# Kernel tuning notes

Hardware: AMD Instinct MI355X
Metric: run time of the kernel (lower is better)

The kernel has to match this reference:

```python
import jax, jax.numpy as jnp
import numpy as np

LOG2 = float(np.log(2.0))

def _ssp(x):
    # shifted softplus: ln(0.5*(exp(x)+1)) = softplus(x) - ln 2
    return jax.nn.softplus(x) - LOG2

def setup_inputs() -> dict:
    key = jax.random.key(0)
    ks = jax.random.split(key, 8)
    B, N, D = 32, 512, 1024
    H = D // 2
    s = lambda fan_in: 1.0 / np.sqrt(fan_in)
    return {
        "representation": jax.random.normal(ks[0], (B, N, D), jnp.float32),
        "R": jax.random.normal(ks[1], (B, N, 3), jnp.float32),
        "atom_mask": jnp.ones((B, N), jnp.float32),
        "W1": jax.random.normal(ks[2], (D, H), jnp.float32) * s(D),
        "b1": jnp.zeros((H,), jnp.float32),
        "W2": jax.random.normal(ks[3], (H, 1), jnp.float32) * s(H),
        "b2": jnp.zeros((1,), jnp.float32),
        "Wc1": jax.random.normal(ks[4], (D, H), jnp.float32) * s(D),
        "bc1": jnp.zeros((H,), jnp.float32),
        "Wc2": jax.random.normal(ks[5], (H, 1), jnp.float32) * s(H),
        "bc2": jnp.zeros((1,), jnp.float32),
    }

def reference(representation, R, atom_mask, W1, b1, W2, b2, Wc1, bc1, Wc2, bc2):
    B, N, _ = representation.shape
    # Atomwise pyramidal MLP: n_in -> n_in//2 (shifted softplus) -> 1
    yi = _ssp(jnp.einsum("bnd,dh->bnh", representation, W1) + b1)
    yi = jnp.einsum("bnh,ho->bno", yi, W2) + b2            # [B,N,1]
    # masked sum pool over atoms (mean=0, stddev=1 so standardize is identity)
    y = jnp.sum(yi * atom_mask[..., None], axis=1)          # [B,1]

    # pairwise distances with safe sqrt (diag is exactly zero)
    diff = R[:, None, :, :] - R[:, :, None, :]              # [B,N,N,3]
    d2 = jnp.sum(diff * diff, axis=-1)                      # [B,N,N]
    dist = jnp.where(d2 > 0, jnp.sqrt(jnp.where(d2 > 0, d2, 1.0)), 0.0)

    eye = jnp.eye(N, dtype=dist.dtype)
    tot_mask = atom_mask[:, None, :] * atom_mask[:, :, None] * (1.0 - eye)
    keep = (tot_mask != 0).astype(dist.dtype)               # [B,N,N]
    dist = dist * keep

    # charge net: Dense(n_in, n_in//2, ssp) -> Dense(n_in//2, 1)
    q = _ssp(jnp.einsum("bnd,dh->bnh", representation, Wc1) + bc1)
    q = jnp.einsum("bnh,ho->bno", q, Wc2) + bc2             # [B,N,1]

    inv2 = (1e-5 + dist) ** -2                              # [B,N,N]
    coulomb = q[:, :, 0][:, None, :] * inv2 * q             # [B,N,N] (q_j * inv * q_i)
    coulomb = coulomb * keep
    e = jnp.sum(coulomb, axis=(1, 2))                       # [B]

    return y + e[:, None]                                   # [B,1]
```

## Files before the change

### kernel.cpp

```cpp
#include <hip/hip_runtime.h>
#include <math.h>


typedef unsigned short u16;
typedef unsigned int u32;
typedef __bf16 bf16x8 __attribute__((ext_vector_type(8)));
typedef float f32x4 __attribute__((ext_vector_type(4)));

#define GK 1024
#define NT 16

#define GLOAD_LDS16(g, l) __builtin_amdgcn_global_load_lds( \
    (const __attribute__((address_space(1))) void*)(g),     \
    (__attribute__((address_space(3))) void*)(l), 16, 0, 0)

__device__ __forceinline__ u16 f2bf(float f) {
    u32 u = __float_as_uint(f);
    return (u16)((u + 0x7FFFu + ((u >> 16) & 1u)) >> 16);
}

__device__ __forceinline__ float ssp_f(float x) {
    return __logf(0.5f * (__expf(x) + 1.0f));
}

__device__ __forceinline__ float ssp_slow(float x) {
    return fmaxf(x, 0.0f) + log1pf(expf(-fabsf(x))) - 0.6931471805599453f;
}


__global__ __launch_bounds__(256) void prep(
    const float* __restrict__ rep, const float* __restrict__ W1,
    const float* __restrict__ Wc1, u16* __restrict__ Abf,
    u16* __restrict__ Btb, float* __restrict__ out)
{
    __shared__ float tile[32][33];
    const int blk = blockIdx.x;
    const int t = threadIdx.x;
    if (blk < 8192) {
        int i = (blk * 256 + t) * 8;
        float4 x = *(const float4*)(rep + i);
        float4 y = *(const float4*)(rep + i + 4);
        union { u16 h[8]; uint4 v; } o;
        o.h[0] = f2bf(x.x); o.h[1] = f2bf(x.y); o.h[2] = f2bf(x.z); o.h[3] = f2bf(x.w);
        o.h[4] = f2bf(y.x); o.h[5] = f2bf(y.y); o.h[6] = f2bf(y.z); o.h[7] = f2bf(y.w);
        *(uint4*)(Abf + i) = o.v;
        if (blk == 0 && t < 32) out[t] = 0.0f;
    } else {
        const int bb = blk - 8192;
        const int k0 = (bb & 31) * 32;
        const int n0 = (bb >> 5) * 32;
        const float* src = (n0 < 512) ? W1 : Wc1;
        const int ns0 = (n0 < 512) ? n0 : n0 - 512;
#pragma unroll
        for (int j = 0; j < 4; j++) {
            int idx = j * 256 + t;
            int kl = idx >> 5, nl = idx & 31;
            tile[kl][nl] = src[(size_t)(k0 + kl) * 512 + ns0 + nl];
        }
        __syncthreads();
#pragma unroll
        for (int j = 0; j < 4; j++) {
            int idx = j * 256 + t;
            int nl = idx >> 5, kl = idx & 31;
            Btb[(size_t)(n0 + nl) * 1024 + k0 + kl] = f2bf(tile[kl][nl]);
        }
    }
}


__global__ __launch_bounds__(512, 2) void gemm_mfma(
    const u16* __restrict__ A,
    const u16* __restrict__ Bt,
    const float* __restrict__ b1, const float* __restrict__ W2,
    const float* __restrict__ bc1, const float* __restrict__ Wc2,
    float* __restrict__ parts)
{
    __shared__ u16 smem[2][16384];

    const int blk = blockIdx.x;
    const int swz = ((blk & 7) << 5) | (blk >> 3);
    const int bm = swz >> 2;
    const int bn = swz & 3;
    const int tid = threadIdx.x;
    const int w = tid >> 6, lane = tid & 63;
    const int wm = w & 1, wn = w >> 1;
    const int lm = lane & 15, q = lane >> 4;

    f32x4 acc[8][4];
#pragma unroll
    for (int i = 0; i < 8; i++)
#pragma unroll
        for (int j = 0; j < 4; j++)
            acc[i][j] = (f32x4){0.0f, 0.0f, 0.0f, 0.0f};

    int goff[2][2];
#pragma unroll
    for (int h = 0; h < 2; h++)
#pragma unroll
        for (int p2 = 0; p2 < 2; p2++) {
            int ci = h * 1024 + (w * 2 + p2) * 64 + lane;
            int row = ci >> 3;
            int c = (ci & 7) ^ (row & 7);
            goff[h][p2] = row * GK + c * 8;
        }

    int arow[4], aswz[2];
#pragma unroll
    for (int mi = 0; mi < 4; mi++) arow[mi] = (wm * 128 + mi * 16 + lm) * 64;
#pragma unroll
    for (int kk = 0; kk < 2; kk++) aswz[kk] = ((kk * 4 + q) ^ (lm & 7)) * 8;

    const u16* Ab = A + (size_t)bm * 256 * GK;
    const u16* Bw = Bt + (size_t)(bn * 256 + wn * 64 + lm) * GK + q * 8;

#define STAGE_A(G, H, BUF) do {                                               \
    GLOAD_LDS16((G) + goff[H][0], &smem[BUF][((H) * 1024 + (w * 2 + 0) * 64) * 8]); \
    GLOAD_LDS16((G) + goff[H][1], &smem[BUF][((H) * 1024 + (w * 2 + 1) * 64) * 8]); \
} while (0)

#define LOAD_B(DST, KT)                                                       \
    _Pragma("unroll") for (int nj = 0; nj < 4; nj++)                          \
    _Pragma("unroll") for (int kk = 0; kk < 2; kk++)                          \
        DST[nj][kk] = *(const bf16x8*)&Bw[(size_t)nj * 16 * GK + (KT) + kk * 32];

#define READ_A(BUF, MH)                                                       \
    _Pragma("unroll") for (int mi = 0; mi < 4; mi++)                          \
    _Pragma("unroll") for (int kk = 0; kk < 2; kk++)                          \
        afr[mi][kk] = *(const bf16x8*)&smem[BUF][arow[mi] + (MH) * 4096 + aswz[kk]];

#define MFMA_HALF(MH, BF)                                                     \
    _Pragma("unroll") for (int kk = 0; kk < 2; kk++)                          \
    _Pragma("unroll") for (int mi = 0; mi < 4; mi++)                          \
    _Pragma("unroll") for (int nj = 0; nj < 4; nj++)                          \
        acc[(MH) * 4 + mi][nj] = __builtin_amdgcn_mfma_f32_16x16x32_bf16(     \
            afr[mi][kk], BF[nj][kk], acc[(MH) * 4 + mi][nj], 0, 0, 0);

#define TILE_BODY(CUR, BCUR, BNXT, TNEXT_KT) do {                             \
    const u16* gA_ = Ab + (TNEXT_KT);                                         \
    STAGE_A(gA_, 0, (CUR) ^ 1);                                               \
    STAGE_A(gA_, 1, (CUR) ^ 1);                                               \
    LOAD_B(BNXT, (TNEXT_KT));                                                 \
    READ_A(CUR, 0);                                                           \
    __builtin_amdgcn_s_setprio(1);                                            \
    MFMA_HALF(0, BCUR);                                                       \
    __builtin_amdgcn_s_setprio(0);                                            \
    READ_A(CUR, 1);                                                           \
    __builtin_amdgcn_s_setprio(1);                                            \
    MFMA_HALF(1, BCUR);                                                       \
    __builtin_amdgcn_s_setprio(0);                                            \
    asm volatile("s_waitcnt vmcnt(0) lgkmcnt(0)" ::: "memory");               \
    __builtin_amdgcn_s_barrier();                                             \
} while (0)

    bf16x8 afr[4][2], bA[4][2], bB[4][2];

    STAGE_A(Ab, 0, 0);
    STAGE_A(Ab, 1, 0);
    LOAD_B(bA, 0);
    asm volatile("s_waitcnt vmcnt(0)" ::: "memory");
    __builtin_amdgcn_s_barrier();

    for (int tt = 0; tt < NT / 2; ++tt) {
        const int t0 = 2 * tt, t1 = 2 * tt + 1;
        TILE_BODY(0, bA, bB, (((t0 + 1) & (NT - 1)) * 64));
        TILE_BODY(1, bB, bA, (((t1 + 1) & (NT - 1)) * 64));
    }

#undef STAGE_A
#undef LOAD_B
#undef READ_A
#undef MFMA_HALF
#undef TILE_BODY

    __syncthreads();
    float* red = (float*)&smem[0][0];
    const bool is_q = (bn >= 2);
    const float* bb2 = is_q ? bc1 : b1;
    const float* vv = is_q ? Wc2 : W2;
    float bias[4], v[4];
#pragma unroll
    for (int nfr = 0; nfr < 4; nfr++) {
        int c = (bn & 1) * 256 + wn * 64 + nfr * 16 + lm;
        bias[nfr] = bb2[c];
        v[nfr] = vv[c];
    }
#pragma unroll
    for (int mfr = 0; mfr < 8; mfr++) {
#pragma unroll
        for (int r = 0; r < 4; r++) {
            float s = 0.0f;
#pragma unroll
            for (int nfr = 0; nfr < 4; nfr++)
                s += v[nfr] * ssp_f(acc[mfr][nfr][r] + bias[nfr]);
            s += __shfl_xor(s, 1);
            s += __shfl_xor(s, 2);
            s += __shfl_xor(s, 4);
            s += __shfl_xor(s, 8);
            if (lm == 0) red[wn * 256 + wm * 128 + mfr * 16 + q * 4 + r] = s;
        }
    }
    __syncthreads();
    if (tid < 256) {
        float val = red[0 * 256 + tid] + red[1 * 256 + tid] +
                    red[2 * 256 + tid] + red[3 * 256 + tid];
        parts[(size_t)bn * 16384 + bm * 256 + tid] = val;
    }
}


__global__ __launch_bounds__(256) void coulomb_k(
    const float* __restrict__ R, const float* __restrict__ mask,
    const float* __restrict__ parts, const float* __restrict__ b2p,
    const float* __restrict__ bc2p, float* __restrict__ out)
{
    const int N = 512;
    const int b = blockIdx.y;
    const int chunk = blockIdx.x;
    __shared__ float Rx[512], Ry[512], Rz[512], QM[512];
    __shared__ float rbuf[4];
    const int tid = threadIdx.x;
    const float bc2 = bc2p[0];
    const float b2 = b2p[0];

    for (int j = tid; j < N; j += 256) {
        int idx = b * N + j;
        float m = mask[idx];
        const float* rp = R + (size_t)idx * 3;
        Rx[j] = rp[0];
        Ry[j] = rp[1];
        Rz[j] = rp[2];
        float qv = parts[2 * 16384 + idx] + parts[3 * 16384 + idx] + bc2;
        QM[j] = qv * m;
    }
    __syncthreads();

    const int i = chunk * 64 + (tid & 63);
    const int js = (tid >> 6) * 128;
    const float xi = Rx[i], yi = Ry[i], zi = Rz[i], qmi = QM[i];
    float e = 0.0f;
    for (int j = js; j < js + 128; j++) {
        float dx = xi - Rx[j];
        float dy = yi - Ry[j];
        float dz = zi - Rz[j];
        float d2 = dx * dx + dy * dy + dz * dz;
        float t = 1e-5f + sqrtf(d2);
        float term = qmi * QM[j] / (t * t);
        e += (j == i) ? 0.0f : term;
    }
    if (tid < 64) {
        int ii = b * N + chunk * 64 + tid;
        float yv = parts[0 * 16384 + ii] + parts[1 * 16384 + ii] + b2;
        e += yv * mask[ii];
    }
    for (int off = 32; off > 0; off >>= 1) e += __shfl_down(e, off, 64);
    if ((tid & 63) == 0) rbuf[tid >> 6] = e;
    __syncthreads();
    if (tid == 0) atomicAdd(&out[b], rbuf[0] + rbuf[1] + rbuf[2] + rbuf[3]);
}


#define BM 128
#define BN 64
#define BK 16

__global__ __launch_bounds__(256) void mlp_gemm(
    const float* __restrict__ A, const float* __restrict__ W1,
    const float* __restrict__ Wc1, const float* __restrict__ b1,
    const float* __restrict__ bc1, const float* __restrict__ W2,
    const float* __restrict__ Wc2, float* __restrict__ yi_part,
    float* __restrict__ q_part)
{
    const int K = 1024;
    const int bm = blockIdx.x;
    const int bn = blockIdx.y;
    const bool is_q = (bn >= 8);
    const float* __restrict__ W = is_q ? Wc1 : W1;
    const int j0 = (bn & 7) * BN;

    __shared__ float As[BK][BM + 4];
    __shared__ float Bs[BK][BN + 4];
    __shared__ float red[BM];

    const int tid = threadIdx.x;
    const int tx = tid & 15;
    const int ty = tid >> 4;

    float acc[8][4];
#pragma unroll
    for (int r = 0; r < 8; r++)
#pragma unroll
        for (int c = 0; c < 4; c++) acc[r][c] = 0.0f;

    const int a_row = tid >> 2;
    const int a_k4 = (tid & 3) * 4;
    const float* Arow0 = A + (size_t)(bm * BM + a_row) * K;
    const float* Arow1 = Arow0 + (size_t)64 * K;
    const int w_k = tid >> 4;
    const int w_j = (tid & 15) * 4;

    for (int kt = 0; kt < K; kt += BK) {
        float4 av0 = *(const float4*)(Arow0 + kt + a_k4);
        float4 av1 = *(const float4*)(Arow1 + kt + a_k4);
        float4 wv = *(const float4*)(W + (size_t)(kt + w_k) * 512 + j0 + w_j);
        __syncthreads();
        As[a_k4 + 0][a_row] = av0.x;
        As[a_k4 + 1][a_row] = av0.y;
        As[a_k4 + 2][a_row] = av0.z;
        As[a_k4 + 3][a_row] = av0.w;
        As[a_k4 + 0][a_row + 64] = av1.x;
        As[a_k4 + 1][a_row + 64] = av1.y;
        As[a_k4 + 2][a_row + 64] = av1.z;
        As[a_k4 + 3][a_row + 64] = av1.w;
        *(float4*)&Bs[w_k][w_j] = wv;
        __syncthreads();
#pragma unroll
        for (int kk = 0; kk < BK; kk++) {
            float4 a0 = *(const float4*)&As[kk][ty * 8];
            float4 a1 = *(const float4*)&As[kk][ty * 8 + 4];
            float4 bv = *(const float4*)&Bs[kk][tx * 4];
            float ar[8] = {a0.x, a0.y, a0.z, a0.w, a1.x, a1.y, a1.z, a1.w};
            float bc[4] = {bv.x, bv.y, bv.z, bv.w};
#pragma unroll
            for (int r = 0; r < 8; r++)
#pragma unroll
                for (int c = 0; c < 4; c++)
                    acc[r][c] = fmaf(ar[r], bc[c], acc[r][c]);
        }
    }

    const float* bb = is_q ? bc1 : b1;
    const float* vv = is_q ? Wc2 : W2;
    float bias[4], v[4];
#pragma unroll
    for (int c = 0; c < 4; c++) {
        bias[c] = bb[j0 + tx * 4 + c];
        v[c] = vv[j0 + tx * 4 + c];
    }
    if (tid < BM) red[tid] = 0.0f;
    __syncthreads();
#pragma unroll
    for (int r = 0; r < 8; r++) {
        float s = 0.0f;
#pragma unroll
        for (int c = 0; c < 4; c++)
            s += v[c] * ssp_slow(acc[r][c] + bias[c]);
        atomicAdd(&red[ty * 8 + r], s);
    }
    __syncthreads();
    float* target = is_q ? q_part : yi_part;
    if (tid < BM) atomicAdd(&target[(size_t)bm * BM + tid], red[tid]);
}

__global__ __launch_bounds__(256) void coulomb_fb(
    const float* __restrict__ R, const float* __restrict__ mask,
    const float* __restrict__ yi_part, const float* __restrict__ q_part,
    const float* __restrict__ b2p, const float* __restrict__ bc2p,
    float* __restrict__ out)
{
    const int N = 512;
    const int b = blockIdx.y;
    const int chunk = blockIdx.x;
    __shared__ float Rx[512], Ry[512], Rz[512], QM[512];
    __shared__ float rbuf[4];
    const int tid = threadIdx.x;
    const float bc2 = bc2p[0];
    const float b2 = b2p[0];

    for (int j = tid; j < N; j += 256) {
        float m = mask[b * N + j];
        const float* rp = R + ((size_t)b * N + j) * 3;
        Rx[j] = rp[0];
        Ry[j] = rp[1];
        Rz[j] = rp[2];
        QM[j] = (q_part[b * N + j] + bc2) * m;
    }
    __syncthreads();

    const int i = chunk * 64 + (tid & 63);
    const int js = (tid >> 6) * 128;
    const float xi = Rx[i], yi = Ry[i], zi = Rz[i], qmi = QM[i];
    float e = 0.0f;
    for (int j = js; j < js + 128; j++) {
        float dx = xi - Rx[j];
        float dy = yi - Ry[j];
        float dz = zi - Rz[j];
        float d2 = dx * dx + dy * dy + dz * dz;
        float t = 1e-5f + sqrtf(d2);
        float term = qmi * QM[j] / (t * t);
        e += (j == i) ? 0.0f : term;
    }
    if (tid < 64) {
        int ii = chunk * 64 + tid;
        e += (yi_part[b * N + ii] + b2) * mask[b * N + ii];
    }
    for (int off = 32; off > 0; off >>= 1) e += __shfl_down(e, off, 64);
    if ((tid & 63) == 0) rbuf[tid >> 6] = e;
    __syncthreads();
    if (tid == 0) atomicAdd(&out[b], rbuf[0] + rbuf[1] + rbuf[2] + rbuf[3]);
}


extern "C" void kernel_launch(void* const* d_in, const int* in_sizes, int n_in,
                              void* d_out, int out_size, void* d_ws, size_t ws_size,
                              hipStream_t stream) {
    const float* rep  = (const float*)d_in[0];
    const float* R    = (const float*)d_in[1];
    const float* mask = (const float*)d_in[2];
    const float* W1   = (const float*)d_in[3];
    const float* b1   = (const float*)d_in[4];
    const float* W2   = (const float*)d_in[5];
    const float* b2   = (const float*)d_in[6];
    const float* Wc1  = (const float*)d_in[7];
    const float* bc1  = (const float*)d_in[8];
    const float* Wc2  = (const float*)d_in[9];
    const float* bc2  = (const float*)d_in[10];
    float* out = (float*)d_out;

    const size_t szA = 16384ull * 1024 * 2;
    const size_t szB = 1024ull * 1024 * 2;
    const size_t szP = 8ull * 16384 * 4;
    const size_t need = szA + szB + szP;

    if (ws_size >= need) {
        u16* Abf = (u16*)d_ws;
        u16* Btb = (u16*)((char*)d_ws + szA);
        float* parts = (float*)((char*)d_ws + szA + szB);

        prep<<<8192 + 1024, 256, 0, stream>>>(rep, W1, Wc1, Abf, Btb, out);
        gemm_mfma<<<256, 512, 0, stream>>>(Abf, Btb, b1, W2, bc1, Wc2, parts);
        coulomb_k<<<dim3(8, 32), 256, 0, stream>>>(R, mask, parts, b2, bc2, out);
    } else {
        float* yi_part = (float*)d_ws;
        float* q_part = yi_part + 16384;
        hipMemsetAsync(d_ws, 0, 2 * 16384 * sizeof(float), stream);
        hipMemsetAsync(d_out, 0, 32 * sizeof(float), stream);
        mlp_gemm<<<dim3(128, 16), 256, 0, stream>>>(rep, W1, Wc1, b1, bc1, W2, Wc2,
                                                    yi_part, q_part);
        coulomb_fb<<<dim3(8, 32), 256, 0, stream>>>(R, mask, yi_part, q_part, b2, bc2, out);
    }
}
```

Baseline: 188.5 us.

## Stage B operand through LDS and pipeline GEMM in quarter-tile phases

The MFMA GEMM now loads the B tile into LDS with async global-to-LDS copies instead of per-wave direct global register loads, and doubles shared memory to hold A and B double buffers. The K-tile body is split into three phases with fine-grained vmcnt/lgkmcnt waits, inline ds_read_b128 with immediate offsets, and barriers, so LDS reads and MFMAs overlap the next tile's staging. The goal is to cut redundant global traffic for B and hide latency. In exchange it uses 128 KB of LDS per block, which may limit occupancy below the declared two blocks per CU, and adds more barriers per tile.

```diff
diff --git a/kernel.cpp b/kernel.cpp
--- a/kernel.cpp
+++ b/kernel.cpp
@@ -75,7 +75,7 @@
     const float* __restrict__ bc1, const float* __restrict__ Wc2,
     float* __restrict__ parts)
 {
-    __shared__ u16 smem[2][16384];
+    __shared__ u16 smem[2][32768];
 
     const int blk = blockIdx.x;
     const int swz = ((blk & 7) << 5) | (blk >> 3);
@@ -93,84 +93,139 @@
         for (int j = 0; j < 4; j++)
             acc[i][j] = (f32x4){0.0f, 0.0f, 0.0f, 0.0f};
 
-    int goff[2][2];
+    int goffA[2][2], goffB[2][2];
 #pragma unroll
     for (int h = 0; h < 2; h++)
 #pragma unroll
         for (int p2 = 0; p2 < 2; p2++) {
             int ci = h * 1024 + (w * 2 + p2) * 64 + lane;
-            int row = ci >> 3;
-            int c = (ci & 7) ^ (row & 7);
-            goff[h][p2] = row * GK + c * 8;
+            int s = ci >> 3;
+            int c = (ci & 7) ^ (s & 7);
+            int gA = (s & 63) + ((s >> 6) & 1) * 128 + ((s >> 7) & 1) * 64;
+            int gB = (s & 31) + ((s >> 5) & 3) * 64 + ((s >> 7) & 1) * 32;
+            goffA[h][p2] = gA * GK + c * 8;
+            goffB[h][p2] = gB * GK + c * 8;
         }
 
-    int arow[4], aswz[2];
-#pragma unroll
-    for (int mi = 0; mi < 4; mi++) arow[mi] = (wm * 128 + mi * 16 + lm) * 64;
-#pragma unroll
-    for (int kk = 0; kk < 2; kk++) aswz[kk] = ((kk * 4 + q) ^ (lm & 7)) * 8;
+    const int aswz0 = (q ^ (lm & 7)) * 8;
+    const int aswz1 = ((4 + q) ^ (lm & 7)) * 8;
+    const u32 base0 = (u32)(size_t)(__attribute__((address_space(3))) void*)&smem[0][0];
+    const u32 aA0 = base0 + 2u * (u32)((wm * 64 + lm) * 64 + aswz0);
+    const u32 aA1 = base0 + 2u * (u32)((wm * 64 + lm) * 64 + aswz1);
+    const u32 bB0 = base0 + 32768u + 2u * (u32)((wn * 32 + lm) * 64 + aswz0);
+    const u32 bB1 = base0 + 32768u + 2u * (u32)((wn * 32 + lm) * 64 + aswz1);
+    const u32 aA0b = aA0 + 65536u, aA1b = aA1 + 65536u;
+    const u32 bB0b = bB0 + 65536u, bB1b = bB1 + 65536u;
 
     const u16* Ab = A + (size_t)bm * 256 * GK;
-    const u16* Bw = Bt + (size_t)(bn * 256 + wn * 64 + lm) * GK + q * 8;
-
-#define STAGE_A(G, H, BUF) do {                                               \
-    GLOAD_LDS16((G) + goff[H][0], &smem[BUF][((H) * 1024 + (w * 2 + 0) * 64) * 8]); \
-    GLOAD_LDS16((G) + goff[H][1], &smem[BUF][((H) * 1024 + (w * 2 + 1) * 64) * 8]); \
+    const u16* Bb = Bt + (size_t)bn * 256 * GK;
+
+#define STAGE2(G, RG, H, BUF, GOFF) do {                                      \
+    GLOAD_LDS16((G) + GOFF[H][0], &smem[BUF][(RG) + ((H) * 1024 + (w * 2 + 0) * 64) * 8]); \
+    GLOAD_LDS16((G) + GOFF[H][1], &smem[BUF][(RG) + ((H) * 1024 + (w * 2 + 1) * 64) * 8]); \
 } while (0)
 
-#define LOAD_B(DST, KT)                                                       \
-    _Pragma("unroll") for (int nj = 0; nj < 4; nj++)                          \
-    _Pragma("unroll") for (int kk = 0; kk < 2; kk++)                          \
-        DST[nj][kk] = *(const bf16x8*)&Bw[(size_t)nj * 16 * GK + (KT) + kk * 32];
-
-#define READ_A(BUF, MH)                                                       \
-    _Pragma("unroll") for (int mi = 0; mi < 4; mi++)                          \
-    _Pragma("unroll") for (int kk = 0; kk < 2; kk++)                          \
-        afr[mi][kk] = *(const bf16x8*)&smem[BUF][arow[mi] + (MH) * 4096 + aswz[kk]];
-
-#define MFMA_HALF(MH, BF)                                                     \
+#define DSR(D, AD, O) asm volatile("ds_read_b128 %0, %1 offset:" #O          \
+                                   : "=v"(D) : "v"(AD))
+
+#define RD_A0(F, R0, R1) do {                                                 \
+    DSR(F[0][0], R0, 0);     DSR(F[0][1], R1, 0);                             \
+    DSR(F[1][0], R0, 2048);  DSR(F[1][1], R1, 2048);                          \
+    DSR(F[2][0], R0, 4096);  DSR(F[2][1], R1, 4096);                          \
+    DSR(F[3][0], R0, 6144);  DSR(F[3][1], R1, 6144); } while (0)
+
+#define RD_A1(F, R0, R1) do {                                                 \
+    DSR(F[0][0], R0, 16384); DSR(F[0][1], R1, 16384);                         \
+    DSR(F[1][0], R0, 18432); DSR(F[1][1], R1, 18432);                         \
+    DSR(F[2][0], R0, 20480); DSR(F[2][1], R1, 20480);                         \
+    DSR(F[3][0], R0, 22528); DSR(F[3][1], R1, 22528); } while (0)
+
+#define RD_B0(F, R0, R1) do {                                                 \
+    DSR(F[0][0], R0, 0);     DSR(F[0][1], R1, 0);                             \
+    DSR(F[1][0], R0, 2048);  DSR(F[1][1], R1, 2048); } while (0)
+
+#define RD_B1(F, R0, R1) do {                                                 \
+    DSR(F[0][0], R0, 16384); DSR(F[0][1], R1, 16384);                         \
+    DSR(F[1][0], R0, 18432); DSR(F[1][1], R1, 18432); } while (0)
+
+#define MFMA_Q(MH, NH, AF, BF)                                                \
     _Pragma("unroll") for (int kk = 0; kk < 2; kk++)                          \
     _Pragma("unroll") for (int mi = 0; mi < 4; mi++)                          \
-    _Pragma("unroll") for (int nj = 0; nj < 4; nj++)                          \
-        acc[(MH) * 4 + mi][nj] = __builtin_amdgcn_mfma_f32_16x16x32_bf16(     \
-            afr[mi][kk], BF[nj][kk], acc[(MH) * 4 + mi][nj], 0, 0, 0);
-
-#define TILE_BODY(CUR, BCUR, BNXT, TNEXT_KT) do {                             \
-    const u16* gA_ = Ab + (TNEXT_KT);                                         \
-    STAGE_A(gA_, 0, (CUR) ^ 1);                                               \
-    STAGE_A(gA_, 1, (CUR) ^ 1);                                               \
-    LOAD_B(BNXT, (TNEXT_KT));                                                 \
-    READ_A(CUR, 0);                                                           \
+    _Pragma("unroll") for (int nj = 0; nj < 2; nj++)                          \
+        acc[(MH) * 4 + mi][(NH) * 2 + nj] = __builtin_amdgcn_mfma_f32_16x16x32_bf16( \
+            AF[mi][kk], BF[nj][kk], acc[(MH) * 4 + mi][(NH) * 2 + nj], 0, 0, 0);
+
+#define WAITV4 do { asm volatile("s_waitcnt vmcnt(4)" ::: "memory");          \
+                    __builtin_amdgcn_sched_barrier(0); } while (0)
+#define LGKM0  do { asm volatile("s_waitcnt lgkmcnt(0)" ::: "memory");        \
+                    __builtin_amdgcn_sched_barrier(0); } while (0)
+
+#define TILE(RA0, RA1, RB0, RB1, SB, GAN, GBN) do {                           \
+                                                                 \
+    STAGE2(GAN, 0, 0, SB, goffA);                                             \
+    RD_A0(afr, RA0, RA1);                                                     \
+    RD_B0(b0f, RB0, RB1);                                                     \
+    __builtin_amdgcn_s_barrier();                                             \
+    LGKM0;                                                                    \
     __builtin_amdgcn_s_setprio(1);                                            \
-    MFMA_HALF(0, BCUR);                                                       \
+    MFMA_Q(0, 0, afr, b0f);                                                   \
     __builtin_amdgcn_s_setprio(0);                                            \
-    READ_A(CUR, 1);                                                           \
+    WAITV4;                                                                   \
+    __builtin_amdgcn_s_barrier();                                             \
+                                                                 \
+    STAGE2(GBN, 16384, 0, SB, goffB);                                         \
+    RD_B1(b1f, RB0, RB1);                                                     \
+    __builtin_amdgcn_s_barrier();                                             \
+    LGKM0;                                                                    \
     __builtin_amdgcn_s_setprio(1);                                            \
-    MFMA_HALF(1, BCUR);                                                       \
+    MFMA_Q(0, 1, afr, b1f);                                                   \
     __builtin_amdgcn_s_setprio(0);                                            \
-    asm volatile("s_waitcnt vmcnt(0) lgkmcnt(0)" ::: "memory");               \
+    WAITV4;                                                                   \
+    __builtin_amdgcn_s_barrier();                                             \
+                                                           \
+    STAGE2(GBN, 16384, 1, SB, goffB);                                         \
+    STAGE2(GAN, 0, 1, SB, goffA);                                             \
+    RD_A1(afr, RA0, RA1);                                                     \
+    __builtin_amdgcn_s_barrier();                                             \
+    LGKM0;                                                                    \
+    __builtin_amdgcn_s_setprio(1);                                            \
+    MFMA_Q(1, 1, afr, b1f);                                                   \
+    MFMA_Q(1, 0, afr, b0f);                                                   \
+    __builtin_amdgcn_s_setprio(0);                                            \
+    WAITV4;                                                                   \
     __builtin_amdgcn_s_barrier();                                             \
 } while (0)
 
-    bf16x8 afr[4][2], bA[4][2], bB[4][2];
-
-    STAGE_A(Ab, 0, 0);
-    STAGE_A(Ab, 1, 0);
-    LOAD_B(bA, 0);
+    bf16x8 afr[4][2], b0f[2][2], b1f[2][2];
+
+    STAGE2(Ab, 0, 0, 0, goffA);
+    STAGE2(Bb, 16384, 0, 0, goffB);
+    STAGE2(Bb, 16384, 1, 0, goffB);
+    STAGE2(Ab, 0, 1, 0, goffA);
+    WAITV4;
+    __builtin_amdgcn_s_barrier();
+
+    for (int tt = 0; tt < 8; ++tt) {
+        const u16* gA0 = Ab + ((2 * tt + 1) & (NT - 1)) * 64;
+        const u16* gB0 = Bb + ((2 * tt + 1) & (NT - 1)) * 64;
+        const u16* gA1 = Ab + ((2 * tt + 2) & (NT - 1)) * 64;
+        const u16* gB1 = Bb + ((2 * tt + 2) & (NT - 1)) * 64;
+        TILE(aA0, aA1, bB0, bB1, 1, gA0, gB0);
+        TILE(aA0b, aA1b, bB0b, bB1b, 0, gA1, gB1);
+    }
+
     asm volatile("s_waitcnt vmcnt(0)" ::: "memory");
-    __builtin_amdgcn_s_barrier();
-
-    for (int tt = 0; tt < NT / 2; ++tt) {
-        const int t0 = 2 * tt, t1 = 2 * tt + 1;
-        TILE_BODY(0, bA, bB, (((t0 + 1) & (NT - 1)) * 64));
-        TILE_BODY(1, bB, bA, (((t1 + 1) & (NT - 1)) * 64));
-    }
-
-#undef STAGE_A
-#undef LOAD_B
-#undef READ_A
-#undef MFMA_HALF
-#undef TILE_BODY
+
+#undef STAGE2
+#undef DSR
+#undef RD_A0
+#undef RD_A1
+#undef RD_B0
+#undef RD_B1
+#undef MFMA_Q
+#undef WAITV4
+#undef LGKM0
+#undef TILE
 
     __syncthreads();
     float* red = (float*)&smem[0][0];
@@ -315,10 +370,10 @@
         __syncthreads();
 #pragma unroll
         for (int kk = 0; kk < BK; kk++) {
-            float4 a0 = *(const float4*)&As[kk][ty * 8];
-            float4 a1 = *(const float4*)&As[kk][ty * 8 + 4];
+            float4 a0v = *(const float4*)&As[kk][ty * 8];
+            float4 a1v = *(const float4*)&As[kk][ty * 8 + 4];
             float4 bv = *(const float4*)&Bs[kk][tx * 4];
-            float ar[8] = {a0.x, a0.y, a0.z, a0.w, a1.x, a1.y, a1.z, a1.w};
+            float ar[8] = {a0v.x, a0v.y, a0v.z, a0v.w, a1v.x, a1v.y, a1v.z, a1v.w};
             float bc[4] = {bv.x, bv.y, bv.z, bv.w};
 #pragma unroll
             for (int r = 0; r < 8; r++)
```

Result: faster. 168.5 us (-10.6%).
